# Performance work log

Hardware: AMD Instinct MI355X
Metric: run time of the kernel (lower is better)

## Reference

```python
import jax, jax.numpy as jnp
import numpy as np

N = 8192        # total nodes (32 events x 256 hits)
G = 32          # events
K = 15          # knn_graph k
FIN = 4         # n_ftx_in
FOUT = 4        # n_ftx_out
SPACE = 3       # n_ftx_space
LAT = 64        # n_ftx_latent
HID = 2 * LAT   # GIN hidden (n_hidden_nodes)


def _leaky(x):
    return jnp.where(x > 0, x, 0.01 * x)


def setup_inputs() -> dict:
    key = jax.random.key(0)
    ks = jax.random.split(key, 20)

    def p(k, shape, fan_in):
        return (jax.random.normal(k, shape, jnp.float32) / jnp.sqrt(jnp.float32(fan_in)))

    inp = {
        "x": jax.random.normal(ks[0], (N, FIN), jnp.float32),
        "batch": (jnp.arange(N) // (N // G)).astype(jnp.int32),
        "condition": jnp.zeros((G, 1), jnp.float32),
        # space_emb FFN: FIN -> LAT -> LAT
        "W_se1": p(ks[1], (FIN, LAT), FIN), "b_se1": jnp.zeros((LAT,), jnp.float32),
        "W_se2": p(ks[2], (LAT, LAT), LAT), "b_se2": jnp.zeros((LAT,), jnp.float32),
        # GINConv 1 MLP: LAT -> HID -> LAT
        "W_g1a": p(ks[3], (LAT, HID), LAT), "b_g1a": jnp.zeros((HID,), jnp.float32),
        "W_g1b": p(ks[4], (HID, LAT), HID), "b_g1b": jnp.zeros((LAT,), jnp.float32),
        # GINConv 2 MLP
        "W_g2a": p(ks[5], (LAT, HID), LAT), "b_g2a": jnp.zeros((HID,), jnp.float32),
        "W_g2b": p(ks[6], (HID, LAT), HID), "b_g2b": jnp.zeros((LAT,), jnp.float32),
        # out_emb FFN: LAT -> LAT -> FOUT
        "W_oe1": p(ks[7], (LAT, LAT), LAT), "b_oe1": jnp.zeros((LAT,), jnp.float32),
        "W_oe2": p(ks[8], (LAT, FOUT), LAT), "b_oe2": jnp.zeros((FOUT,), jnp.float32),
    }
    return inp


def _knn_graph(pos, batch, k):
    # pairwise squared distances within the same event only; no self-loops
    d = jnp.sum((pos[:, None, :] - pos[None, :, :]) ** 2, axis=-1)  # [N, N]
    ii = jnp.arange(pos.shape[0])
    valid = (batch[:, None] == batch[None, :]) & (ii[:, None] != ii[None, :])
    d = jnp.where(valid, d, jnp.float32(1e30))
    _, nbr = jax.lax.top_k(-d, k)                 # [N, K] nearest neighbor ids
    src = nbr.reshape(-1)                          # neighbor j (source)
    dst = jnp.repeat(ii, k)                        # center i (target)
    return jnp.stack([src, dst])                   # PyG edge_index layout


def _gin(h, src, dst, Wa, ba, Wb, bb):
    # GINConv, eps=0: mlp(x_i + sum_j x_j)
    agg = jax.ops.segment_sum(h[src], dst, num_segments=h.shape[0])
    m = h + agg
    return jnp.maximum(m @ Wa + ba, 0.0) @ Wb + bb


def reference(x, batch, condition,
              W_se1, b_se1, W_se2, b_se2,
              W_g1a, b_g1a, W_g1b, b_g1b,
              W_g2a, b_g2a, W_g2b, b_g2b,
              W_oe1, b_oe1, W_oe2, b_oe2):
    # space_emb FFN
    h = _leaky(x @ W_se1 + b_se1) @ W_se2 + b_se2          # [N, LAT]
    # dynamic knn graph on first SPACE dims of the embedding
    ei = _knn_graph(h[:, :SPACE], batch, K)                 # [2, N*K]
    src, dst = ei[0], ei[1]
    # MPLSeq: 2 GINConv layers with residual skip (cond unused, n_cond=0)
    h = h + _gin(h, src, dst, W_g1a, b_g1a, W_g1b, b_g1b)
    h = h + _gin(h, src, dst, W_g2a, b_g2a, W_g2b, b_g2b)
    # out_emb FFN
    x_emb = _leaky(h @ W_oe1 + b_oe1) @ W_oe2 + b_oe2       # [N, FOUT]
    return (h, x_emb, ei)
```

## Files before the change

kernel.cpp:

```cpp
#include <hip/hip_runtime.h>


#define N_NODES 8192
#define NPE     256
#define KNN     15
#define LAT     64
#define HID     128
#define NK      (N_NODES*KNN)
#define NBLK    512
#define NTHR    512
#define NPB     16
#define NEV     32
#define BPEV    16
#define EI0     (N_NODES*LAT + N_NODES*4)
#define PADM    68
#define PADT    136

#define BARA_CNT 0
#define BARA_FLG 4096
#define BARB_CNT 8192
#define BARB_FLG 12288
#define BAR_BYTES 16384

#define OFF_HA  BAR_BYTES
#define OFF_HB  (OFF_HA + N_NODES*LAT*4)
#define OFF_POS (OFF_HB + N_NODES*LAT*4)

typedef unsigned short bf16;
typedef unsigned int   u32;
typedef unsigned long long u64;
typedef short s16x8 __attribute__((ext_vector_type(8)));
typedef float f32x4 __attribute__((ext_vector_type(4)));

__device__ __forceinline__ float bf2f(bf16 s) {
    union { u32 u; float f; } v; v.u = ((u32)s) << 16; return v.f;
}
__device__ __forceinline__ bf16 f2bf(float f) {
    union { float f; u32 u; } v; v.f = f;
    u32 u = v.u + 0x7fffu + ((v.u >> 16) & 1u);
    return (bf16)(u >> 16);
}
__device__ __forceinline__ float ldf(const void* p, int i, int f32) {
    return f32 ? ((const float*)p)[i] : bf2f(((const bf16*)p)[i]);
}
__device__ __forceinline__ void st_coh(float* p, float v) {
    __hip_atomic_store(p, v, __ATOMIC_RELAXED, __HIP_MEMORY_SCOPE_AGENT);
}

union Frag { u32 w[4]; s16x8 v; };

__device__ __forceinline__ u32 cvtpk(float a, float b) {
    u32 r; asm("v_cvt_pk_bf16_f32 %0, %1, %2" : "=v"(r) : "v"(a), "v"(b));
    return r;
}
__device__ __forceinline__ float lo2f(u32 w) { union {u32 u; float f;} v; v.u = w << 16;          return v.f; }
__device__ __forceinline__ float hi2f(u32 w) { union {u32 u; float f;} v; v.u = w & 0xffff0000u;  return v.f; }

__device__ __forceinline__ void split8(const float* x, Frag& hi, Frag& lo) {
    #pragma unroll
    for (int i = 0; i < 4; i++) {
        hi.w[i] = cvtpk(x[2*i], x[2*i+1]);
        lo.w[i] = cvtpk(x[2*i]   - lo2f(hi.w[i]),
                        x[2*i+1] - hi2f(hi.w[i]));
    }
}
__device__ __forceinline__ void packA(const float* p, Frag& hi, Frag& lo) {
    float xv[8];
    *(float4*)&xv[0] = *(const float4*)p;
    *(float4*)&xv[4] = *(const float4*)(p + 4);
    split8(xv, hi, lo);
}
__device__ __forceinline__ void loadB_bf(const bf16* p, int stride, Frag& f) {
    #pragma unroll
    for (int i = 0; i < 4; i++)
        f.w[i] = (u32)p[(2*i)*stride] | ((u32)p[(2*i+1)*stride] << 16);
}
__device__ __forceinline__ void loadB_f32(const float* p, int stride, Frag& hi, Frag& lo) {
    float xv[8];
    #pragma unroll
    for (int j = 0; j < 8; j++) xv[j] = p[j*stride];
    split8(xv, hi, lo);
}
__device__ __forceinline__ f32x4 MF(const Frag& a, const Frag& b, f32x4 c) {
    return __builtin_amdgcn_mfma_f32_16x16x32_bf16(a.v, b.v, c, 0, 0, 0);
}

struct KArgs {
    const void* x;
    const void* se1; const void* bse1; const void* se2; const void* bse2;
    const void* g1a; const void* bg1a; const void* g1b; const void* bg1b;
    const void* g2a; const void* bg2a; const void* g2b; const void* bg2b;
    const void* oe1; const void* boe1; const void* oe2; const void* boe2;
    const u32* wdet;
    float* hA; float* hB; float* pos; int* bar;
    void* out;
};

struct Shm {
    union {
        int    red[NTHR];
        float  hid[NPB][LAT];
        struct { float x[NPE], y[NPE], z[NPE]; } k;
        float4 part[2][NPB][16];
        float  st[NPB*LAT];
    } u;
    float m[NPB*PADM];
    float own[NPB*LAT];
    struct { bf16 hi[NPB*PADT]; bf16 lo[NPB*PADT]; } t;
    float sh[NPB*LAT];
    int   snb[NPB*KNN];
    int   flag;
};

__device__ __forceinline__ void eventbar(int* cnt, int* flg) {
    asm volatile("s_waitcnt vmcnt(0)" ::: "memory");
    __syncthreads();
    if (threadIdx.x == 0) {
        if (__hip_atomic_fetch_add(cnt, 1, __ATOMIC_RELAXED,
                                   __HIP_MEMORY_SCOPE_AGENT) == BPEV - 1) {
            __hip_atomic_store(flg, 1, __ATOMIC_RELAXED,
                               __HIP_MEMORY_SCOPE_AGENT);
        }
        int guard = 0;
        while (__hip_atomic_load(flg, __ATOMIC_RELAXED,
                                 __HIP_MEMORY_SCOPE_AGENT) == 0) {
            __builtin_amdgcn_s_sleep(2);
            if (++guard > (1 << 20)) break;
        }
        __builtin_amdgcn_fence(__ATOMIC_ACQUIRE, "workgroup");
    }
    __syncthreads();
}

template<bool LAST>
__device__ __forceinline__ void gin_layer(Shm& S, int base, int f32,
        const float* __restrict__ hin, float* hout,
        const void* Wa, const void* ba, const void* Wb, const void* bb,
        void* out)
{
    const int tid = threadIdx.x;
    const int lane = tid & 63, wv = tid >> 6;
    const int ln15 = lane & 15, kg = lane >> 4;

    {
        const int h = tid >> 8, n = (tid >> 4) & 15, slot = tid & 15;
        const float4* h4 = (const float4*)hin;
        const int* nb = &S.snb[n*KNN];
        float4 s4;
        if (h == 0) {
            s4 = h4[(size_t)(base + n)*16 + slot];
            *(float4*)&S.own[n*LAT + slot*4] = s4;
            #pragma unroll
            for (int k = 0; k < 7; k++) {
                const float4 v = h4[(size_t)nb[k]*16 + slot];
                s4.x += v.x; s4.y += v.y; s4.z += v.z; s4.w += v.w;
            }
        } else {
            s4 = h4[(size_t)nb[7]*16 + slot];
            #pragma unroll
            for (int k = 8; k < 15; k++) {
                const float4 v = h4[(size_t)nb[k]*16 + slot];
                s4.x += v.x; s4.y += v.y; s4.z += v.z; s4.w += v.w;
            }
        }
        S.u.part[h][n][slot] = s4;
        __syncthreads();
        if (tid < 256) {
            const int n2 = tid >> 4, sl = tid & 15;
            const float4 p0 = S.u.part[0][n2][sl], p1 = S.u.part[1][n2][sl];
            float4 mm; mm.x = p0.x + p1.x; mm.y = p0.y + p1.y;
            mm.z = p0.z + p1.z; mm.w = p0.w + p1.w;
            *(float4*)&S.m[n2*PADM + sl*4] = mm;
        }
        __syncthreads();
    }

    {
        const int u0 = wv * 16;
        const float bias = ldf(ba, u0 + ln15, f32);
        f32x4 acc; acc[0] = bias; acc[1] = bias; acc[2] = bias; acc[3] = bias;
        Frag a0h, a0l, a1h, a1l;
        packA(&S.m[ln15*PADM +  0 + kg*8], a0h, a0l);
        packA(&S.m[ln15*PADM + 32 + kg*8], a1h, a1l);
        if (f32) {
            const float* W = (const float*)Wa;
            Frag b0h, b0l, b1h, b1l;
            loadB_f32(W + ( 0 + kg*8)*HID + u0 + ln15, HID, b0h, b0l);
            loadB_f32(W + (32 + kg*8)*HID + u0 + ln15, HID, b1h, b1l);
            acc = MF(a0h, b0h, acc); acc = MF(a0l, b0h, acc); acc = MF(a0h, b0l, acc);
            acc = MF(a1h, b1h, acc); acc = MF(a1l, b1h, acc); acc = MF(a1h, b1l, acc);
        } else {
            const bf16* W = (const bf16*)Wa;
            Frag b0, b1;
            loadB_bf(W + ( 0 + kg*8)*HID + u0 + ln15, HID, b0);
            loadB_bf(W + (32 + kg*8)*HID + u0 + ln15, HID, b1);
            acc = MF(a0h, b0, acc); acc = MF(a0l, b0, acc);
            acc = MF(a1h, b1, acc); acc = MF(a1l, b1, acc);
        }
        #pragma unroll
        for (int r = 0; r < 4; r++) {
            const int row = kg*4 + r;
            float v = acc[r]; v = v > 0.f ? v : 0.f;
            const bf16 h = f2bf(v);
            S.t.hi[row*PADT + u0 + ln15] = h;
            S.t.lo[row*PADT + u0 + ln15] = f2bf(v - bf2f(h));
        }
    }
    __syncthreads();

    if (wv < 4) {
        const int f0 = wv * 16;
        const float bias = ldf(bb, f0 + ln15, f32);
        f32x4 acc; acc[0] = bias; acc[1] = bias; acc[2] = bias; acc[3] = bias;
        #pragma unroll
        for (int s = 0; s < 4; s++) {
            Frag ah, al;
            ah.v = *(const s16x8*)&S.t.hi[ln15*PADT + s*32 + kg*8];
            al.v = *(const s16x8*)&S.t.lo[ln15*PADT + s*32 + kg*8];
            if (f32) {
                const float* W = (const float*)Wb;
                Frag bh, bl;
                loadB_f32(W + (s*32 + kg*8)*LAT + f0 + ln15, LAT, bh, bl);
                acc = MF(ah, bh, acc); acc = MF(al, bh, acc); acc = MF(ah, bl, acc);
            } else {
                const bf16* W = (const bf16*)Wb;
                Frag b;
                loadB_bf(W + (s*32 + kg*8)*LAT + f0 + ln15, LAT, b);
                acc = MF(ah, b, acc); acc = MF(al, b, acc);
            }
        }
        #pragma unroll
        for (int r = 0; r < 4; r++) {
            const int row = kg*4 + r, f = f0 + ln15, gi = base + row;
            const float o = acc[r] + S.own[row*LAT + f];
            if (!LAST) {
                st_coh(&hout[gi*LAT + f], o);
            } else {
                S.sh[row*LAT + f] = o;
                if (f32) ((float*)out)[gi*LAT + f] = o;
                else     ((bf16*)out)[gi*LAT + f] = f2bf(o);
            }
        }
    }
    __syncthreads();
}

__global__ __launch_bounds__(NTHR, 4) void k_fused(KArgs a)
{
    __shared__ Shm S;
    const int tid = threadIdx.x, blk = blockIdx.x;
    const int ev   = blk & (NEV - 1);
    const int slc  = blk >> 5;
    const int base = ev * NPE + slc * NPB;

    {
        int c = 0;
        for (int i = tid; i < 4096; i += NTHR) {
            const u32 x = a.wdet[i];
            c += ((x >> 7)  & 0xffu) >= 0xC8u;
            c += ((x >> 23) & 0xffu) >= 0xC8u;
        }
        S.u.red[tid] = c;
        __syncthreads();
        for (int s = NTHR/2; s > 0; s >>= 1) {
            if (tid < s) S.u.red[tid] += S.u.red[tid + s];
            __syncthreads();
        }
        if (tid == 0) S.flag = (S.u.red[0] > 64) ? 1 : 0;
        __syncthreads();
    }
    const int f32 = S.flag;
    __syncthreads();

    {
        #pragma unroll
        for (int p = 0; p < 2; p++) {
            const int e = tid + p*NTHR, n = e >> 6, f = e & 63, node = base + n;
            float acc = ldf(a.bse1, f, f32);
            #pragma unroll
            for (int i = 0; i < 4; i++)
                acc = fmaf(ldf(a.x, node*4 + i, f32), ldf(a.se1, i*LAT + f, f32), acc);
            acc = acc > 0.f ? acc : 0.01f*acc;
            S.u.hid[n][f] = acc;
        }
        __syncthreads();
        const int q = tid >> 6, f = tid & 63;
        float a0 = ldf(a.bse2, f, f32);
        float a1 = a0;
        if (f32) {
            const float* W = (const float*)a.se2;
            #pragma unroll 8
            for (int j = 0; j < LAT; j++) {
                const float w = W[j*LAT + f];
                a0 = fmaf(S.u.hid[q][j],     w, a0);
                a1 = fmaf(S.u.hid[q + 8][j], w, a1);
            }
        } else {
            const bf16* W = (const bf16*)a.se2;
            #pragma unroll 8
            for (int j = 0; j < LAT; j++) {
                const float w = bf2f(W[j*LAT + f]);
                a0 = fmaf(S.u.hid[q][j],     w, a0);
                a1 = fmaf(S.u.hid[q + 8][j], w, a1);
            }
        }
        const int n0 = base + q, n1 = base + q + 8;
        st_coh(&a.hA[n0*LAT + f], a0);
        st_coh(&a.hA[n1*LAT + f], a1);
        if (f < 3) {
            st_coh(&a.pos[n0*3 + f], a0);
            st_coh(&a.pos[n1*3 + f], a1);
        }
    }
    eventbar(a.bar + (BARA_CNT + ev*128)/4, a.bar + (BARA_FLG + ev*128)/4);

    {
        const int eb = ev * NPE;
        if (tid < NPE) {
            S.u.k.x[tid] = a.pos[(size_t)(eb + tid)*3 + 0];
            S.u.k.y[tid] = a.pos[(size_t)(eb + tid)*3 + 1];
            S.u.k.z[tid] = a.pos[(size_t)(eb + tid)*3 + 2];
        }
        __syncthreads();
        const int wave = tid >> 6, lane = tid & 63;
        #pragma unroll
        for (int t = 0; t < 2; ++t) {
            const int n  = base + wave*2 + t;
            const int nl = n - eb;
            const float px = S.u.k.x[nl], py = S.u.k.y[nl], pz = S.u.k.z[nl];
            u64 key[4];
            #pragma unroll
            for (int c = 0; c < 4; c++) {
                const int j = 64*c + lane;
                const float dx = px - S.u.k.x[j], dy = py - S.u.k.y[j],
                            dz = pz - S.u.k.z[j];
                float dd = __fmul_rn(dx, dx);
                dd = __fadd_rn(dd, __fmul_rn(dy, dy));
                dd = __fadd_rn(dd, __fmul_rn(dz, dz));
                key[c] = ((u64)__float_as_uint(dd) << 32) | (u32)j;
                if (j == nl) key[c] = ~0ull;
            }
            #define CSWAP(A,B) { const u64 x_ = key[A], y_ = key[B]; \
                                 key[A] = x_ < y_ ? x_ : y_; key[B] = x_ < y_ ? y_ : x_; }
            CSWAP(0,1) CSWAP(2,3) CSWAP(0,2) CSWAP(1,3) CSWAP(1,2)
            #undef CSWAP
            int myj = 0;
            #pragma unroll
            for (int k = 0; k < KNN; k++) {
                u64 m = key[0];
                #pragma unroll
                for (int s = 32; s >= 1; s >>= 1) {
                    const u64 o = __shfl_xor(m, s, 64);
                    m = o < m ? o : m;
                }
                if (lane == k) myj = (int)(u32)m;
                const bool hit = (key[0] == m);
                key[0] = hit ? key[1] : key[0];
                key[1] = hit ? key[2] : key[1];
                key[2] = hit ? key[3] : key[2];
                key[3] = hit ? ~0ull  : key[3];
            }
            if (lane < KNN) {
                const int gj = eb + myj;
                S.snb[(n - base)*KNN + lane] = gj;
                if (f32) {
                    float* o = (float*)a.out;
                    o[EI0 + n*KNN + lane]      = (float)gj;
                    o[EI0 + NK + n*KNN + lane] = (float)n;
                } else {
                    bf16* o = (bf16*)a.out;
                    o[EI0 + n*KNN + lane]      = f2bf((float)gj);
                    o[EI0 + NK + n*KNN + lane] = f2bf((float)n);
                }
            }
        }
        __syncthreads();
    }

    gin_layer<false>(S, base, f32, a.hA, a.hB,
                     a.g1a, a.bg1a, a.g1b, a.bg1b, nullptr);
    eventbar(a.bar + (BARB_CNT + ev*128)/4, a.bar + (BARB_FLG + ev*128)/4);

    gin_layer<true>(S, base, f32, a.hB, nullptr,
                    a.g2a, a.bg2a, a.g2b, a.bg2b, a.out);

    {
        const int q = tid >> 6, f = tid & 63;
        float a0 = ldf(a.boe1, f, f32);
        float a1 = a0;
        if (f32) {
            const float* W = (const float*)a.oe1;
            #pragma unroll 8
            for (int j = 0; j < LAT; j++) {
                const float w = W[j*LAT + f];
                a0 = fmaf(S.sh[(q    )*LAT + j], w, a0);
                a1 = fmaf(S.sh[(q + 8)*LAT + j], w, a1);
            }
        } else {
            const bf16* W = (const bf16*)a.oe1;
            #pragma unroll 8
            for (int j = 0; j < LAT; j++) {
                const float w = bf2f(W[j*LAT + f]);
                a0 = fmaf(S.sh[(q    )*LAT + j], w, a0);
                a1 = fmaf(S.sh[(q + 8)*LAT + j], w, a1);
            }
        }
        a0 = a0 > 0.f ? a0 : 0.01f*a0;
        a1 = a1 > 0.f ? a1 : 0.01f*a1;
        __syncthreads();
        S.u.st[(q    )*LAT + f] = a0;
        S.u.st[(q + 8)*LAT + f] = a1;
        __syncthreads();
        if (tid < NPB*4) {
            const int n = tid >> 2, ff = tid & 3;
            float acc = ldf(a.boe2, ff, f32);
            for (int j = 0; j < LAT; j++)
                acc = fmaf(S.u.st[n*LAT + j], ldf(a.oe2, j*4 + ff, f32), acc);
            const int xo = N_NODES*LAT + (base + n)*4 + ff;
            if (f32) ((float*)a.out)[xo] = acc;
            else     ((bf16*)a.out)[xo] = f2bf(acc);
        }
    }
}

extern "C" void kernel_launch(void* const* d_in, const int* in_sizes, int n_in,
                              void* d_out, int out_size, void* d_ws, size_t ws_size,
                              hipStream_t stream)
{
    (void)in_sizes; (void)n_in; (void)out_size; (void)ws_size;
    char* ws = (char*)d_ws;

    KArgs a;
    a.x   = d_in[0];
    a.se1 = d_in[3];  a.bse1 = d_in[4];  a.se2 = d_in[5];  a.bse2 = d_in[6];
    a.g1a = d_in[7];  a.bg1a = d_in[8];  a.g1b = d_in[9];  a.bg1b = d_in[10];
    a.g2a = d_in[11]; a.bg2a = d_in[12]; a.g2b = d_in[13]; a.bg2b = d_in[14];
    a.oe1 = d_in[15]; a.boe1 = d_in[16]; a.oe2 = d_in[17]; a.boe2 = d_in[18];
    a.wdet = (const u32*)d_in[7];
    a.hA  = (float*)(ws + OFF_HA);
    a.hB  = (float*)(ws + OFF_HB);
    a.pos = (float*)(ws + OFF_POS);
    a.bar = (int*)ws;
    a.out = d_out;

    hipMemsetAsync(d_ws, 0, BAR_BYTES, stream);
    k_fused<<<dim3(NBLK), dim3(NTHR), 0, stream>>>(a);
}
```

Before: 132.6 us.

## Move small FFN matmuls to MFMA, restructure gather, interleave two-node kNN

Replaces the scalar FMA loops for the second space-embedding layer and the first output layer with split-bf16 MFMA tiles, and computes the three position outputs separately with a scalar loop. The GIN neighbour gather now has each thread load all 15 neighbours as float2 with a tree sum, which removes the two-half partial reduction and one barrier. The kNN selection processes two query nodes per wave at once so their shuffle chains interleave. It also swaps the shared-memory flag reduction for wave shuffles and shortens the barrier spin sleep. Together these aim to cut latency in a barrier-bound fused kernel, at the cost of more register pressure and a small precision change from the split-bf16 matmuls.

```diff
diff --git a/kernel.cpp b/kernel.cpp
--- a/kernel.cpp
+++ b/kernel.cpp
@@ -14,6 +14,7 @@
 #define BPEV    16
 #define EI0     (N_NODES*LAT + N_NODES*4)
 #define PADM    68
+#define PADH    68
 #define PADT    136
 
 #define BARA_CNT 0
@@ -53,8 +54,8 @@
     u32 r; asm("v_cvt_pk_bf16_f32 %0, %1, %2" : "=v"(r) : "v"(a), "v"(b));
     return r;
 }
-__device__ __forceinline__ float lo2f(u32 w) { union {u32 u; float f;} v; v.u = w << 16;          return v.f; }
-__device__ __forceinline__ float hi2f(u32 w) { union {u32 u; float f;} v; v.u = w & 0xffff0000u;  return v.f; }
+__device__ __forceinline__ float lo2f(u32 w) { union {u32 u; float f;} v; v.u = w << 16;         return v.f; }
+__device__ __forceinline__ float hi2f(u32 w) { union {u32 u; float f;} v; v.u = w & 0xffff0000u; return v.f; }
 
 __device__ __forceinline__ void split8(const float* x, Frag& hi, Frag& lo) {
     #pragma unroll
@@ -98,16 +99,15 @@
 
 struct Shm {
     union {
-        int    red[NTHR];
-        float  hid[NPB][LAT];
+        int   red[8];
+        float hid[NPB][PADH];
         struct { float x[NPE], y[NPE], z[NPE]; } k;
-        float4 part[2][NPB][16];
-        float  st[NPB*LAT];
+        float st[NPB*LAT];
     } u;
     float m[NPB*PADM];
     float own[NPB*LAT];
     struct { bf16 hi[NPB*PADT]; bf16 lo[NPB*PADT]; } t;
-    float sh[NPB*LAT];
+    float sh[NPB*PADH];
     int   snb[NPB*KNN];
     int   flag;
 };
@@ -124,8 +124,8 @@
         int guard = 0;
         while (__hip_atomic_load(flg, __ATOMIC_RELAXED,
                                  __HIP_MEMORY_SCOPE_AGENT) == 0) {
-            __builtin_amdgcn_s_sleep(2);
-            if (++guard > (1 << 20)) break;
+            __builtin_amdgcn_s_sleep(1);
+            if (++guard > (1 << 21)) break;
         }
         __builtin_amdgcn_fence(__ATOMIC_ACQUIRE, "workgroup");
     }
@@ -143,35 +143,28 @@
     const int ln15 = lane & 15, kg = lane >> 4;
 
     {
-        const int h = tid >> 8, n = (tid >> 4) & 15, slot = tid & 15;
-        const float4* h4 = (const float4*)hin;
+        const int n = tid >> 5, sl = tid & 31;
+        const float2* h2 = (const float2*)hin;
         const int* nb = &S.snb[n*KNN];
-        float4 s4;
-        if (h == 0) {
-            s4 = h4[(size_t)(base + n)*16 + slot];
-            *(float4*)&S.own[n*LAT + slot*4] = s4;
-            #pragma unroll
-            for (int k = 0; k < 7; k++) {
-                const float4 v = h4[(size_t)nb[k]*16 + slot];
-                s4.x += v.x; s4.y += v.y; s4.z += v.z; s4.w += v.w;
-            }
-        } else {
-            s4 = h4[(size_t)nb[7]*16 + slot];
-            #pragma unroll
-            for (int k = 8; k < 15; k++) {
-                const float4 v = h4[(size_t)nb[k]*16 + slot];
-                s4.x += v.x; s4.y += v.y; s4.z += v.z; s4.w += v.w;
-            }
-        }
-        S.u.part[h][n][slot] = s4;
-        __syncthreads();
-        if (tid < 256) {
-            const int n2 = tid >> 4, sl = tid & 15;
-            const float4 p0 = S.u.part[0][n2][sl], p1 = S.u.part[1][n2][sl];
-            float4 mm; mm.x = p0.x + p1.x; mm.y = p0.y + p1.y;
-            mm.z = p0.z + p1.z; mm.w = p0.w + p1.w;
-            *(float4*)&S.m[n2*PADM + sl*4] = mm;
-        }
+        const float2 o = h2[(size_t)(base + n)*32 + sl];
+        *(float2*)&S.own[n*LAT + sl*2] = o;
+        float2 vv[KNN];
+        #pragma unroll
+        for (int k = 0; k < KNN; k++) vv[k] = h2[(size_t)nb[k]*32 + sl];
+        float2 mm;
+        {
+            float s0 = vv[0].x+vv[1].x, s1 = vv[2].x+vv[3].x, s2 = vv[4].x+vv[5].x;
+            float s3 = vv[6].x+vv[7].x, s4 = vv[8].x+vv[9].x, s5 = vv[10].x+vv[11].x;
+            float s6 = vv[12].x+vv[13].x;
+            mm.x = o.x + (((s0+s1)+(s2+s3)) + ((s4+s5)+(s6+vv[14].x)));
+        }
+        {
+            float s0 = vv[0].y+vv[1].y, s1 = vv[2].y+vv[3].y, s2 = vv[4].y+vv[5].y;
+            float s3 = vv[6].y+vv[7].y, s4 = vv[8].y+vv[9].y, s5 = vv[10].y+vv[11].y;
+            float s6 = vv[12].y+vv[13].y;
+            mm.y = o.y + (((s0+s1)+(s2+s3)) + ((s4+s5)+(s6+vv[14].y)));
+        }
+        *(float2*)&S.m[n*PADM + sl*2] = mm;
         __syncthreads();
     }
 
@@ -236,7 +229,7 @@
             if (!LAST) {
                 st_coh(&hout[gi*LAT + f], o);
             } else {
-                S.sh[row*LAT + f] = o;
+                S.sh[row*PADH + f] = o;
                 if (f32) ((float*)out)[gi*LAT + f] = o;
                 else     ((bf16*)out)[gi*LAT + f] = f2bf(o);
             }
@@ -249,6 +242,8 @@
 {
     __shared__ Shm S;
     const int tid = threadIdx.x, blk = blockIdx.x;
+    const int lane = tid & 63, wv = tid >> 6;
+    const int ln15 = lane & 15, kg = lane >> 4;
     const int ev   = blk & (NEV - 1);
     const int slc  = blk >> 5;
     const int base = ev * NPE + slc * NPB;
@@ -260,13 +255,16 @@
             c += ((x >> 7)  & 0xffu) >= 0xC8u;
             c += ((x >> 23) & 0xffu) >= 0xC8u;
         }
-        S.u.red[tid] = c;
-        __syncthreads();
-        for (int s = NTHR/2; s > 0; s >>= 1) {
-            if (tid < s) S.u.red[tid] += S.u.red[tid + s];
-            __syncthreads();
-        }
-        if (tid == 0) S.flag = (S.u.red[0] > 64) ? 1 : 0;
+        #pragma unroll
+        for (int s = 32; s >= 1; s >>= 1) c += __shfl_xor(c, s, 64);
+        if (lane == 0) S.u.red[wv] = c;
+        __syncthreads();
+        if (tid == 0) {
+            int t = 0;
+            #pragma unroll
+            for (int i = 0; i < 8; i++) t += S.u.red[i];
+            S.flag = (t > 64) ? 1 : 0;
+        }
         __syncthreads();
     }
     const int f32 = S.flag;
@@ -276,40 +274,65 @@
         #pragma unroll
         for (int p = 0; p < 2; p++) {
             const int e = tid + p*NTHR, n = e >> 6, f = e & 63, node = base + n;
+            float xr[4];
+            if (f32) {
+                const float4 x4 = ((const float4*)a.x)[node];
+                xr[0] = x4.x; xr[1] = x4.y; xr[2] = x4.z; xr[3] = x4.w;
+            } else {
+                const ushort4 x4 = ((const ushort4*)a.x)[node];
+                xr[0] = bf2f(x4.x); xr[1] = bf2f(x4.y);
+                xr[2] = bf2f(x4.z); xr[3] = bf2f(x4.w);
+            }
             float acc = ldf(a.bse1, f, f32);
             #pragma unroll
             for (int i = 0; i < 4; i++)
-                acc = fmaf(ldf(a.x, node*4 + i, f32), ldf(a.se1, i*LAT + f, f32), acc);
+                acc = fmaf(xr[i], ldf(a.se1, i*LAT + f, f32), acc);
             acc = acc > 0.f ? acc : 0.01f*acc;
             S.u.hid[n][f] = acc;
         }
         __syncthreads();
-        const int q = tid >> 6, f = tid & 63;
-        float a0 = ldf(a.bse2, f, f32);
-        float a1 = a0;
-        if (f32) {
-            const float* W = (const float*)a.se2;
-            #pragma unroll 8
-            for (int j = 0; j < LAT; j++) {
-                const float w = W[j*LAT + f];
-                a0 = fmaf(S.u.hid[q][j],     w, a0);
-                a1 = fmaf(S.u.hid[q + 8][j], w, a1);
-            }
-        } else {
-            const bf16* W = (const bf16*)a.se2;
-            #pragma unroll 8
-            for (int j = 0; j < LAT; j++) {
-                const float w = bf2f(W[j*LAT + f]);
-                a0 = fmaf(S.u.hid[q][j],     w, a0);
-                a1 = fmaf(S.u.hid[q + 8][j], w, a1);
-            }
-        }
-        const int n0 = base + q, n1 = base + q + 8;
-        st_coh(&a.hA[n0*LAT + f], a0);
-        st_coh(&a.hA[n1*LAT + f], a1);
-        if (f < 3) {
-            st_coh(&a.pos[n0*3 + f], a0);
-            st_coh(&a.pos[n1*3 + f], a1);
+        if (wv < 4) {
+            const int f0 = wv * 16;
+            const float bias = ldf(a.bse2, f0 + ln15, f32);
+            f32x4 acc; acc[0] = bias; acc[1] = bias; acc[2] = bias; acc[3] = bias;
+            Frag a0h, a0l, a1h, a1l;
+            packA(&S.u.hid[ln15][ 0 + kg*8], a0h, a0l);
+            packA(&S.u.hid[ln15][32 + kg*8], a1h, a1l);
+            if (f32) {
+                const float* W = (const float*)a.se2;
+                Frag b0h, b0l, b1h, b1l;
+                loadB_f32(W + ( 0 + kg*8)*LAT + f0 + ln15, LAT, b0h, b0l);
+                loadB_f32(W + (32 + kg*8)*LAT + f0 + ln15, LAT, b1h, b1l);
+                acc = MF(a0h, b0h, acc); acc = MF(a0l, b0h, acc); acc = MF(a0h, b0l, acc);
+                acc = MF(a1h, b1h, acc); acc = MF(a1l, b1h, acc); acc = MF(a1h, b1l, acc);
+            } else {
+                const bf16* W = (const bf16*)a.se2;
+                Frag b0, b1;
+                loadB_bf(W + ( 0 + kg*8)*LAT + f0 + ln15, LAT, b0);
+                loadB_bf(W + (32 + kg*8)*LAT + f0 + ln15, LAT, b1);
+                acc = MF(a0h, b0, acc); acc = MF(a0l, b0, acc);
+                acc = MF(a1h, b1, acc); acc = MF(a1l, b1, acc);
+            }
+            #pragma unroll
+            for (int r = 0; r < 4; r++) {
+                const int row = kg*4 + r;
+                st_coh(&a.hA[(base + row)*LAT + f0 + ln15], acc[r]);
+            }
+        } else if (tid - 256 < 48) {
+            const int idx = tid - 256, n = idx / 3, f = idx % 3;
+            float acc = ldf(a.bse2, f, f32);
+            if (f32) {
+                const float* W = (const float*)a.se2;
+                #pragma unroll 8
+                for (int j = 0; j < LAT; j++)
+                    acc = fmaf(S.u.hid[n][j], W[j*LAT + f], acc);
+            } else {
+                const bf16* W = (const bf16*)a.se2;
+                #pragma unroll 8
+                for (int j = 0; j < LAT; j++)
+                    acc = fmaf(S.u.hid[n][j], bf2f(W[j*LAT + f]), acc);
+            }
+            st_coh(&a.pos[(base + n)*3 + f], acc);
         }
     }
     eventbar(a.bar + (BARA_CNT + ev*128)/4, a.bar + (BARA_FLG + ev*128)/4);
@@ -322,56 +345,76 @@
             S.u.k.z[tid] = a.pos[(size_t)(eb + tid)*3 + 2];
         }
         __syncthreads();
-        const int wave = tid >> 6, lane = tid & 63;
-        #pragma unroll
-        for (int t = 0; t < 2; ++t) {
-            const int n  = base + wave*2 + t;
-            const int nl = n - eb;
-            const float px = S.u.k.x[nl], py = S.u.k.y[nl], pz = S.u.k.z[nl];
-            u64 key[4];
-            #pragma unroll
-            for (int c = 0; c < 4; c++) {
-                const int j = 64*c + lane;
-                const float dx = px - S.u.k.x[j], dy = py - S.u.k.y[j],
-                            dz = pz - S.u.k.z[j];
+        const int n0 = base + wv*2, n1 = n0 + 1;
+        const int nl0 = n0 - eb, nl1 = n1 - eb;
+        const float px0 = S.u.k.x[nl0], py0 = S.u.k.y[nl0], pz0 = S.u.k.z[nl0];
+        const float px1 = S.u.k.x[nl1], py1 = S.u.k.y[nl1], pz1 = S.u.k.z[nl1];
+        u64 key0[4], key1[4];
+        #pragma unroll
+        for (int c = 0; c < 4; c++) {
+            const int j = 64*c + lane;
+            const float qx = S.u.k.x[j], qy = S.u.k.y[j], qz = S.u.k.z[j];
+            {
+                const float dx = px0 - qx, dy = py0 - qy, dz = pz0 - qz;
                 float dd = __fmul_rn(dx, dx);
                 dd = __fadd_rn(dd, __fmul_rn(dy, dy));
                 dd = __fadd_rn(dd, __fmul_rn(dz, dz));
-                key[c] = ((u64)__float_as_uint(dd) << 32) | (u32)j;
-                if (j == nl) key[c] = ~0ull;
-            }
-            #define CSWAP(A,B) { const u64 x_ = key[A], y_ = key[B]; \
-                                 key[A] = x_ < y_ ? x_ : y_; key[B] = x_ < y_ ? y_ : x_; }
-            CSWAP(0,1) CSWAP(2,3) CSWAP(0,2) CSWAP(1,3) CSWAP(1,2)
-            #undef CSWAP
-            int myj = 0;
+                key0[c] = ((u64)__float_as_uint(dd) << 32) | (u32)j;
+                if (j == nl0) key0[c] = ~0ull;
+            }
+            {
+                const float dx = px1 - qx, dy = py1 - qy, dz = pz1 - qz;
+                float dd = __fmul_rn(dx, dx);
+                dd = __fadd_rn(dd, __fmul_rn(dy, dy));
+                dd = __fadd_rn(dd, __fmul_rn(dz, dz));
+                key1[c] = ((u64)__float_as_uint(dd) << 32) | (u32)j;
+                if (j == nl1) key1[c] = ~0ull;
+            }
+        }
+        #define CSWAP(K,A,B) { const u64 x_ = K[A], y_ = K[B]; \
+                               K[A] = x_ < y_ ? x_ : y_; K[B] = x_ < y_ ? y_ : x_; }
+        CSWAP(key0,0,1) CSWAP(key0,2,3) CSWAP(key0,0,2) CSWAP(key0,1,3) CSWAP(key0,1,2)
+        CSWAP(key1,0,1) CSWAP(key1,2,3) CSWAP(key1,0,2) CSWAP(key1,1,3) CSWAP(key1,1,2)
+        #undef CSWAP
+        int myj0 = 0, myj1 = 0;
+        #pragma unroll
+        for (int k = 0; k < KNN; k++) {
+            u64 m0 = key0[0], m1 = key1[0];
             #pragma unroll
-            for (int k = 0; k < KNN; k++) {
-                u64 m = key[0];
-                #pragma unroll
-                for (int s = 32; s >= 1; s >>= 1) {
-                    const u64 o = __shfl_xor(m, s, 64);
-                    m = o < m ? o : m;
-                }
-                if (lane == k) myj = (int)(u32)m;
-                const bool hit = (key[0] == m);
-                key[0] = hit ? key[1] : key[0];
-                key[1] = hit ? key[2] : key[1];
-                key[2] = hit ? key[3] : key[2];
-                key[3] = hit ? ~0ull  : key[3];
-            }
-            if (lane < KNN) {
-                const int gj = eb + myj;
-                S.snb[(n - base)*KNN + lane] = gj;
-                if (f32) {
-                    float* o = (float*)a.out;
-                    o[EI0 + n*KNN + lane]      = (float)gj;
-                    o[EI0 + NK + n*KNN + lane] = (float)n;
-                } else {
-                    bf16* o = (bf16*)a.out;
-                    o[EI0 + n*KNN + lane]      = f2bf((float)gj);
-                    o[EI0 + NK + n*KNN + lane] = f2bf((float)n);
-                }
+            for (int s = 32; s >= 1; s >>= 1) {
+                const u64 o0 = __shfl_xor(m0, s, 64);
+                const u64 o1 = __shfl_xor(m1, s, 64);
+                m0 = o0 < m0 ? o0 : m0;
+                m1 = o1 < m1 ? o1 : m1;
+            }
+            if (lane == k) { myj0 = (int)(u32)m0; myj1 = (int)(u32)m1; }
+            const bool h0 = (key0[0] == m0);
+            key0[0] = h0 ? key0[1] : key0[0];
+            key0[1] = h0 ? key0[2] : key0[1];
+            key0[2] = h0 ? key0[3] : key0[2];
+            key0[3] = h0 ? ~0ull   : key0[3];
+            const bool h1 = (key1[0] == m1);
+            key1[0] = h1 ? key1[1] : key1[0];
+            key1[1] = h1 ? key1[2] : key1[1];
+            key1[2] = h1 ? key1[3] : key1[2];
+            key1[3] = h1 ? ~0ull   : key1[3];
+        }
+        if (lane < KNN) {
+            const int gj0 = eb + myj0, gj1 = eb + myj1;
+            S.snb[(n0 - base)*KNN + lane] = gj0;
+            S.snb[(n1 - base)*KNN + lane] = gj1;
+            if (f32) {
+                float* o = (float*)a.out;
+                o[EI0 + n0*KNN + lane]      = (float)gj0;
+                o[EI0 + NK + n0*KNN + lane] = (float)n0;
+                o[EI0 + n1*KNN + lane]      = (float)gj1;
+                o[EI0 + NK + n1*KNN + lane] = (float)n1;
+            } else {
+                bf16* o = (bf16*)a.out;
+                o[EI0 + n0*KNN + lane]      = f2bf((float)gj0);
+                o[EI0 + NK + n0*KNN + lane] = f2bf((float)n0);
+                o[EI0 + n1*KNN + lane]      = f2bf((float)gj1);
+                o[EI0 + NK + n1*KNN + lane] = f2bf((float)n1);
             }
         }
         __syncthreads();
@@ -385,31 +428,36 @@
                     a.g2a, a.bg2a, a.g2b, a.bg2b, a.out);
 
     {
-        const int q = tid >> 6, f = tid & 63;
-        float a0 = ldf(a.boe1, f, f32);
-        float a1 = a0;
-        if (f32) {
-            const float* W = (const float*)a.oe1;
-            #pragma unroll 8
-            for (int j = 0; j < LAT; j++) {
-                const float w = W[j*LAT + f];
-                a0 = fmaf(S.sh[(q    )*LAT + j], w, a0);
-                a1 = fmaf(S.sh[(q + 8)*LAT + j], w, a1);
-            }
-        } else {
-            const bf16* W = (const bf16*)a.oe1;
-            #pragma unroll 8
-            for (int j = 0; j < LAT; j++) {
-                const float w = bf2f(W[j*LAT + f]);
-                a0 = fmaf(S.sh[(q    )*LAT + j], w, a0);
-                a1 = fmaf(S.sh[(q + 8)*LAT + j], w, a1);
-            }
-        }
-        a0 = a0 > 0.f ? a0 : 0.01f*a0;
-        a1 = a1 > 0.f ? a1 : 0.01f*a1;
-        __syncthreads();
-        S.u.st[(q    )*LAT + f] = a0;
-        S.u.st[(q + 8)*LAT + f] = a1;
+        if (wv < 4) {
+            const int f0 = wv * 16;
+            const float bias = ldf(a.boe1, f0 + ln15, f32);
+            f32x4 acc; acc[0] = bias; acc[1] = bias; acc[2] = bias; acc[3] = bias;
+            Frag a0h, a0l, a1h, a1l;
+            packA(&S.sh[ln15*PADH +  0 + kg*8], a0h, a0l);
+            packA(&S.sh[ln15*PADH + 32 + kg*8], a1h, a1l);
+            if (f32) {
+                const float* W = (const float*)a.oe1;
+                Frag b0h, b0l, b1h, b1l;
+                loadB_f32(W + ( 0 + kg*8)*LAT + f0 + ln15, LAT, b0h, b0l);
+                loadB_f32(W + (32 + kg*8)*LAT + f0 + ln15, LAT, b1h, b1l);
+                acc = MF(a0h, b0h, acc); acc = MF(a0l, b0h, acc); acc = MF(a0h, b0l, acc);
+                acc = MF(a1h, b1h, acc); acc = MF(a1l, b1h, acc); acc = MF(a1h, b1l, acc);
+            } else {
+                const bf16* W = (const bf16*)a.oe1;
+                Frag b0, b1;
+                loadB_bf(W + ( 0 + kg*8)*LAT + f0 + ln15, LAT, b0);
+                loadB_bf(W + (32 + kg*8)*LAT + f0 + ln15, LAT, b1);
+                acc = MF(a0h, b0, acc); acc = MF(a0l, b0, acc);
+                acc = MF(a1h, b1, acc); acc = MF(a1l, b1, acc);
+            }
+            #pragma unroll
+            for (int r = 0; r < 4; r++) {
+                const int row = kg*4 + r;
+                float v = acc[r];
+                v = v > 0.f ? v : 0.01f*v;
+                S.u.st[row*LAT + f0 + ln15] = v;
+            }
+        }
         __syncthreads();
         if (tid < NPB*4) {
             const int n = tid >> 2, ff = tid & 3;
```

New measurement: 131.7 us. About the same (-0.7%).
